# Optimization experiments

Measured on AMD Instinct MI355X. Metric: run time of the kernel, lower is better.

Reference implementation:

```python
import jax, jax.numpy as jnp
import numpy as np

NU = NI = 100_000  # nodes per ntype
E = 500_000        # edges per metapath graph
M = 2              # metapaths per ntype
D = 64             # in_size == out_size (num_heads = 1)
H = 128            # semantic-attention hidden
B = 8192           # batch of (user, pos, neg) indices
LRELU = 0.2        # DGL GATConv leaky-relu slope
EPS = 1e-5


def setup_inputs() -> dict:
    key = jax.random.key(0)
    ks = iter(jax.random.split(key, 40))
    rn = lambda sh, s=0.1: jax.random.normal(next(ks), sh, jnp.float32) * s
    ri = lambda sh, hi: jax.random.randint(next(ks), sh, 0, hi, jnp.int32)
    return dict(
        user_idx=ri((B,), NU), item_idx=ri((B,), NI), neg_item_idx=ri((B,), NI),
        user_feat=rn((NU, D), 1.0), item_feat=rn((NI, D), 1.0),
        u_src=ri((M, E), NU), u_dst=ri((M, E), NU),
        i_src=ri((M, E), NI), i_dst=ri((M, E), NI),
        u_W=rn((M, D, D)), u_al=rn((M, D)), u_ar=rn((M, D)), u_b=rn((M, D)),
        i_W=rn((M, D, D)), i_al=rn((M, D)), i_ar=rn((M, D)), i_b=rn((M, D)),
        u_saW1=rn((D, H)), u_sab1=rn((H,)), u_saW2=rn((H, 1)),
        i_saW1=rn((D, H)), i_sab1=rn((H,)), i_saW2=rn((H, 1)),
        userW=rn((D, D)), userb=rn((D,)), itemW=rn((D, D)), itemb=rn((D,)),
        ln_g=jnp.ones((D,), jnp.float32), ln_b=jnp.zeros((D,), jnp.float32),
    )


def _gat_stack(h, W, al, ar, b, src, dst, n_nodes):
    # One GATConv (single head) per metapath, vmapped over the metapath axis.
    def one(Wm, alm, arm, bm, s, d):
        feat = h @ Wm                               # (N, D)
        el = feat @ alm                             # (N,)
        er = feat @ arm                             # (N,)
        e = jax.nn.leaky_relu(el[s] + er[d], LRELU)  # (E,)
        m = jax.ops.segment_max(e, d, num_segments=n_nodes)
        ex = jnp.exp(e - m[d])
        den = jax.ops.segment_sum(ex, d, num_segments=n_nodes)
        alpha = ex / (den[d] + 1e-9)                # per-dst edge softmax
        out = jax.ops.segment_sum(alpha[:, None] * feat[s], d, num_segments=n_nodes)
        return jax.nn.elu(out + bm)                 # (N, D)
    return jax.vmap(one)(W, al, ar, b, src, dst)    # (M, N, D)


def _semantic_attention(z, W1, b1, W2):
    # z: (M, N, D) -> (N, D)
    w = jnp.mean(jnp.tanh(jnp.einsum('mnd,dh->mnh', z, W1) + b1) @ W2, axis=1)  # (M, 1)
    beta = jax.nn.softmax(w, axis=0)                 # softmax over metapaths
    return jnp.sum(beta[:, :, None] * z, axis=0)     # (N, D) -- beta (M,1)->(M,1,1)


def _layernorm(x, g, b):
    mu = x.mean(-1, keepdims=True)
    v = ((x - mu) ** 2).mean(-1, keepdims=True)
    return g * (x - mu) / jnp.sqrt(v + EPS) + b


def reference(user_idx, item_idx, neg_item_idx, user_feat, item_feat,
              u_src, u_dst, i_src, i_dst,
              u_W, u_al, u_ar, u_b, i_W, i_al, i_ar, i_b,
              u_saW1, u_sab1, u_saW2, i_saW1, i_sab1, i_saW2,
              userW, userb, itemW, itemb, ln_g, ln_b):
    zu = _gat_stack(user_feat, u_W, u_al, u_ar, u_b, u_src, u_dst, NU)
    zi = _gat_stack(item_feat, i_W, i_al, i_ar, i_b, i_src, i_dst, NI)
    user_emb = _semantic_attention(zu, u_saW1, u_sab1, u_saW2)
    item_emb = _semantic_attention(zi, i_saW1, i_sab1, i_saW2)
    user_emb = _layernorm(jax.nn.relu(user_emb @ userW + userb), ln_g, ln_b)
    item_emb = _layernorm(jax.nn.relu(item_emb @ itemW + itemb), ln_g, ln_b)
    return (user_emb[user_idx], item_emb[item_idx], item_emb[neg_item_idx])
```

## Files before the change

kernel.cpp:

```cpp
#include <hip/hip_runtime.h>
#include <math.h>

#define N_NODES 100000
#define N_EDGES 500000
#define BATCH   8192
#define NBLK    98
#define HISTX   512
#define FEATX   256

typedef __bf16 bf16;
typedef __bf16 bf16x8 __attribute__((ext_vector_type(8)));
typedef float  f32x4  __attribute__((ext_vector_type(4)));

#define MFMA16(a, b, c) __builtin_amdgcn_mfma_f32_16x16x32_bf16((a), (b), (c), 0, 0, 0)

__device__ __forceinline__ float wave_reduce_sum(float v) {
    #pragma unroll
    for (int off = 32; off; off >>= 1) v += __shfl_xor(v, off);
    return v;
}

__device__ __forceinline__ float fast_tanh(float x) {
    float e = __expf(2.f * x);
    return 1.f - 2.f / (e + 1.f);
}

__device__ __forceinline__ float b2f(unsigned short u) {
    return __int_as_float(((int)u) << 16);
}

__global__ void __launch_bounds__(256, 6)
fh_all(const float* __restrict__ uf, const float* __restrict__ itf,
       const float* __restrict__ uW, const float* __restrict__ iW,
       const float* __restrict__ ual, const float* __restrict__ ial,
       const float* __restrict__ uar, const float* __restrict__ iar,
       bf16* __restrict__ feat, float* __restrict__ el, float* __restrict__ er,
       const int* __restrict__ udst, const int* __restrict__ idst,
       int* __restrict__ cnt4, int* __restrict__ rank, int E, int N) {
    __shared__ bf16x8 ldsW[8][64];
    const int g = blockIdx.y;
    if (blockIdx.x < HISTX) {
        const int* dst = ((g < 2) ? udst : idst) + (size_t)(g & 1) * E;
        int* cntg = cnt4 + (size_t)g * N;
        int* rk = rank + (size_t)g * E;
        const int tid = blockIdx.x * blockDim.x + threadIdx.x;
        const int stride = HISTX * blockDim.x;
        for (int i0 = tid; i0 < E; i0 += 4 * stride) {
            const int i1 = i0 + stride, i2 = i0 + 2 * stride, i3 = i0 + 3 * stride;
            int d0 = dst[i0];
            int d1 = (i1 < E) ? dst[i1] : 0;
            int d2 = (i2 < E) ? dst[i2] : 0;
            int d3 = (i3 < E) ? dst[i3] : 0;
            int r0 = 0, r1 = 0, r2 = 0, r3 = 0;
            r0 = atomicAdd(&cntg[(size_t)(i0 & 3) * 4 * N + d0], 1);
            if (i1 < E) r1 = atomicAdd(&cntg[(size_t)(i1 & 3) * 4 * N + d1], 1);
            if (i2 < E) r2 = atomicAdd(&cntg[(size_t)(i2 & 3) * 4 * N + d2], 1);
            if (i3 < E) r3 = atomicAdd(&cntg[(size_t)(i3 & 3) * 4 * N + d3], 1);
            rk[i0] = r0;
            if (i1 < E) rk[i1] = r1;
            if (i2 < E) rk[i2] = r2;
            if (i3 < E) rk[i3] = r3;
        }
        return;
    }
    const int t = g >> 1, m = g & 1;
    const int fx = (int)blockIdx.x - HISTX;
    const float* h   = t ? itf : uf;
    const float* Wm  = (t ? iW : uW) + (size_t)m * 4096;
    const float* alb = (t ? ial : ual) + m * 64;
    const float* arb = (t ? iar : uar) + m * 64;
    for (int f = threadIdx.x; f < 8 * 64; f += blockDim.x) {
        int id = f >> 6, l = f & 63;
        int lc = l & 15, lq = l >> 4;
        int nt = id >> 1, kf = id & 1;
        bf16x8 v;
        #pragma unroll
        for (int j = 0; j < 8; ++j)
            v[j] = (bf16)Wm[(kf * 32 + lq * 8 + j) * 64 + nt * 16 + lc];
        ldsW[id][l] = v;
    }
    __syncthreads();
    const int lane = threadIdx.x & 63, wave = threadIdx.x >> 6, wpb = blockDim.x >> 6;
    const int c = lane & 15, q = lane >> 4;
    float alv[4], arv[4];
    #pragma unroll
    for (int nt = 0; nt < 4; ++nt) {
        alv[nt] = alb[nt * 16 + c];
        arv[nt] = arb[nt * 16 + c];
    }
    const f32x4 zf = {0.f, 0.f, 0.f, 0.f};
    const int tiles = N >> 4;
    bf16* fg   = feat + (size_t)g * N * 64;
    float* elg = el + (size_t)g * N;
    float* erg = er + (size_t)g * N;
    for (int tile = fx * wpb + wave; tile < tiles; tile += FEATX * wpb) {
        const float* hr = h + (size_t)(tile * 16 + c) * 64 + q * 8;
        f32x4 v0 = *(const f32x4*)hr;
        f32x4 v1 = *(const f32x4*)(hr + 4);
        f32x4 v2 = *(const f32x4*)(hr + 32);
        f32x4 v3 = *(const f32x4*)(hr + 36);
        bf16x8 a0, a1;
        #pragma unroll
        for (int j = 0; j < 4; ++j) {
            a0[j] = (bf16)v0[j]; a0[j + 4] = (bf16)v1[j];
            a1[j] = (bf16)v2[j]; a1[j + 4] = (bf16)v3[j];
        }
        f32x4 acc[4];
        #pragma unroll
        for (int nt = 0; nt < 4; ++nt) {
            acc[nt] = zf;
            acc[nt] = MFMA16(a0, ldsW[nt * 2][lane], acc[nt]);
            acc[nt] = MFMA16(a1, ldsW[nt * 2 + 1][lane], acc[nt]);
        }
        #pragma unroll
        for (int nt = 0; nt < 4; ++nt)
            #pragma unroll
            for (int r = 0; r < 4; ++r)
                fg[(size_t)(tile * 16 + q * 4 + r) * 64 + nt * 16 + c] = (bf16)acc[nt][r];
        #pragma unroll
        for (int r = 0; r < 4; ++r) {
            float se = 0.f, sr = 0.f;
            #pragma unroll
            for (int nt = 0; nt < 4; ++nt) {
                se = fmaf(acc[nt][r], alv[nt], se);
                sr = fmaf(acc[nt][r], arv[nt], sr);
            }
            #pragma unroll
            for (int off = 1; off < 16; off <<= 1) {
                se += __shfl_xor(se, off);
                sr += __shfl_xor(sr, off);
            }
            if (c == 0) {
                elg[tile * 16 + q * 4 + r] = se;
                erg[tile * 16 + q * 4 + r] = sr;
            }
        }
    }
}

__global__ void scanA(const int* __restrict__ cnt4, int* __restrict__ offsets,
                      int* __restrict__ bsum, int N) {
    const int g = blockIdx.y;
    const int* c = cnt4 + (size_t)g * N;
    int* o = offsets + (size_t)g * (N + 1);
    __shared__ int sh[1024];
    int i = blockIdx.x * 1024 + (int)threadIdx.x;
    int v = 0;
    if (i < N)
        v = c[i] + c[(size_t)4 * N + i] + c[(size_t)8 * N + i] + c[(size_t)12 * N + i];
    sh[threadIdx.x] = v;
    __syncthreads();
    for (int off = 1; off < 1024; off <<= 1) {
        int tv = (threadIdx.x >= (unsigned)off) ? sh[threadIdx.x - off] : 0;
        __syncthreads();
        sh[threadIdx.x] += tv;
        __syncthreads();
    }
    if (i < N) o[i] = sh[threadIdx.x] - v;
    if (threadIdx.x == 1023) bsum[g * 128 + blockIdx.x] = sh[1023];
}

__global__ void scanB(int* __restrict__ bsum, int* __restrict__ offsets,
                      float* __restrict__ wsum, int N) {
    const int g = blockIdx.y;
    int* bs = bsum + g * 128;
    __shared__ int sh[128];
    int tid = (int)threadIdx.x;
    if (g == 0 && tid < 4) wsum[tid] = 0.f;
    int v = (tid < NBLK) ? bs[tid] : 0;
    sh[tid] = v;
    __syncthreads();
    for (int off = 1; off < 128; off <<= 1) {
        int tv = (tid >= off) ? sh[tid - off] : 0;
        __syncthreads();
        sh[tid] += tv;
        __syncthreads();
    }
    if (tid < NBLK) bs[tid] = sh[tid] - v;
    if (tid == 0) offsets[(size_t)g * (N + 1) + N] = sh[127];
}

__global__ void scanC(int* __restrict__ offsets, int* __restrict__ off4,
                      const int* __restrict__ cnt4, const int* __restrict__ bsum, int N) {
    const int g = blockIdx.y;
    int i = blockIdx.x * blockDim.x + threadIdx.x;
    if (i < N) {
        int base = offsets[(size_t)g * (N + 1) + i] + bsum[g * 128 + (i >> 10)];
        offsets[(size_t)g * (N + 1) + i] = base;
        const int* c = cnt4 + (size_t)g * N;
        int c0 = c[i], c1 = c[(size_t)4 * N + i], c2 = c[(size_t)8 * N + i];
        int4 o;
        o.x = base; o.y = base + c0; o.z = base + c0 + c1; o.w = base + c0 + c1 + c2;
        *(int4*)(off4 + ((size_t)g * N + i) * 4) = o;
    }
}

__global__ void scatter_all(const int* __restrict__ usrc, const int* __restrict__ udst,
                            const int* __restrict__ isrc, const int* __restrict__ idst,
                            const float* __restrict__ el, const float* __restrict__ er,
                            const int* __restrict__ off4, const int* __restrict__ rank,
                            int2* __restrict__ epack, int E, int N) {
    const int g = blockIdx.y;
    const int* src = ((g < 2) ? usrc : isrc) + (size_t)(g & 1) * E;
    const int* dst = ((g < 2) ? udst : idst) + (size_t)(g & 1) * E;
    const float* elg = el + (size_t)g * N;
    const float* erg = er + (size_t)g * N;
    const int* o4 = off4 + (size_t)g * N * 4;
    const int* rk = rank + (size_t)g * E;
    int2* ep = epack + (size_t)g * E;
    const int tid = blockIdx.x * blockDim.x + threadIdx.x;
    const int stride = gridDim.x * blockDim.x;
    for (int i0 = tid; i0 < E; i0 += 4 * stride) {
        #pragma unroll
        for (int u = 0; u < 4; ++u) {
            const int i = i0 + u * stride;
            if (i < E) {
                int s = src[i], d = dst[i];
                int pos = o4[d * 4 + (i & 3)] + rk[i];
                float e = elg[s] + erg[d];
                e = (e >= 0.f) ? e : 0.2f * e;
                ep[pos] = make_int2(s << 7, __float_as_int(__expf(e)));
            }
        }
    }
}

__global__ void agg_all(const unsigned short* __restrict__ feat,
                        const float* __restrict__ ub, const float* __restrict__ ib,
                        const int* __restrict__ offsets, const int2* __restrict__ epack,
                        bf16* __restrict__ z, int E, int N) {
    const int g = blockIdx.y;
    const char* featg = (const char*)(feat + (size_t)g * N * 64);
    const float* bv = ((g < 2) ? ub : ib) + (g & 1) * 64;
    const int* offg = offsets + (size_t)g * (N + 1);
    const int2* ep = epack + (size_t)g * E;
    bf16* zg = z + (size_t)g * N * 64;
    const int lane = threadIdx.x & 63, wave = threadIdx.x >> 6, wpb = blockDim.x >> 6;
    const int lane2 = lane * 2;
    const float bl = bv[lane];
    for (int node0 = blockIdx.x * wpb + wave; node0 < N; node0 += gridDim.x * wpb) {
        const int node = __builtin_amdgcn_readfirstlane(node0);
        const int beg = __builtin_amdgcn_readfirstlane(offg[node]);
        const int end = __builtin_amdgcn_readfirstlane(offg[node + 1]);
        float l = 0.f, acc0 = 0.f, acc1 = 0.f;
        int i = beg;
        for (; i + 4 <= end; i += 4) {
            int2 p0 = ep[i], p1 = ep[i + 1], p2 = ep[i + 2], p3 = ep[i + 3];
            float f0 = b2f(*(const unsigned short*)(featg + (p0.x + lane2)));
            float f1 = b2f(*(const unsigned short*)(featg + (p1.x + lane2)));
            float f2 = b2f(*(const unsigned short*)(featg + (p2.x + lane2)));
            float f3 = b2f(*(const unsigned short*)(featg + (p3.x + lane2)));
            float w0 = __int_as_float(p0.y), w1 = __int_as_float(p1.y);
            float w2 = __int_as_float(p2.y), w3 = __int_as_float(p3.y);
            l += (w0 + w1) + (w2 + w3);
            acc0 = fmaf(w0, f0, acc0);
            acc1 = fmaf(w1, f1, acc1);
            acc0 = fmaf(w2, f2, acc0);
            acc1 = fmaf(w3, f3, acc1);
        }
        for (; i < end; ++i) {
            int2 p = ep[i];
            float w = __int_as_float(p.y);
            l += w;
            acc0 = fmaf(w, b2f(*(const unsigned short*)(featg + (p.x + lane2))), acc0);
        }
        float acc = acc0 + acc1;
        float o = acc / (l + 1e-9f);
        float zz = o + bl;
        zz = (zz > 0.f) ? zz : expm1f(zz);
        zg[(size_t)node * 64 + lane] = (bf16)zz;
    }
}

__global__ void __launch_bounds__(256, 4)
sem_mfma(const bf16* __restrict__ z,
         const float* __restrict__ uW1, const float* __restrict__ iW1,
         const float* __restrict__ ub1, const float* __restrict__ ib1,
         const float* __restrict__ uW2, const float* __restrict__ iW2,
         float* __restrict__ wsum, int N) {
    const int g = blockIdx.y, t = g >> 1;
    const float* W1 = t ? iW1 : uW1;
    const float* b1 = t ? ib1 : ub1;
    const float* W2 = t ? iW2 : uW2;
    __shared__ bf16x8 ldsW[16][64];
    for (int f = threadIdx.x; f < 16 * 64; f += blockDim.x) {
        int id = f >> 6, l = f & 63;
        int lc = l & 15, lq = l >> 4;
        int nt = id >> 1, kf = id & 1;
        bf16x8 v;
        #pragma unroll
        for (int j = 0; j < 8; ++j)
            v[j] = (bf16)W1[(kf * 32 + lq * 8 + j) * 128 + nt * 16 + lc];
        ldsW[id][l] = v;
    }
    __syncthreads();
    const int lane = threadIdx.x & 63, wave = threadIdx.x >> 6, wpb = blockDim.x >> 6;
    const int c = lane & 15, q = lane >> 4;
    float b1v[8], w2v[8];
    #pragma unroll
    for (int nt = 0; nt < 8; ++nt) { b1v[nt] = b1[nt * 16 + c]; w2v[nt] = W2[nt * 16 + c]; }
    const bf16* zg = z + (size_t)g * N * 64;
    const f32x4 zf = {0.f, 0.f, 0.f, 0.f};
    float local = 0.f;
    const int tiles = N >> 4;
    for (int tile = blockIdx.x * wpb + wave; tile < tiles; tile += gridDim.x * wpb) {
        const bf16* zr = zg + (size_t)(tile * 16 + c) * 64;
        bf16x8 a0 = *(const bf16x8*)(zr + q * 8);
        bf16x8 a1 = *(const bf16x8*)(zr + 32 + q * 8);
        f32x4 acc[8];
        #pragma unroll
        for (int nt = 0; nt < 8; ++nt) {
            acc[nt] = zf;
            acc[nt] = MFMA16(a0, ldsW[nt * 2][lane], acc[nt]);
            acc[nt] = MFMA16(a1, ldsW[nt * 2 + 1][lane], acc[nt]);
        }
        #pragma unroll
        for (int nt = 0; nt < 8; ++nt)
            #pragma unroll
            for (int r = 0; r < 4; ++r)
                local += w2v[nt] * fast_tanh(acc[nt][r] + b1v[nt]);
    }
    local = wave_reduce_sum(local);
    if (lane == 0) atomicAdd(&wsum[g], local);
}

__global__ void out_all(const int* __restrict__ uidx, const int* __restrict__ iidx,
                        const int* __restrict__ nidx, const bf16* __restrict__ z,
                        const float* __restrict__ wsum,
                        const float* __restrict__ userW, const float* __restrict__ userb,
                        const float* __restrict__ itemW, const float* __restrict__ itemb,
                        const float* __restrict__ ln_g, const float* __restrict__ ln_b,
                        float* __restrict__ out, int N, int B) {
    const int grp = blockIdx.y;
    const int t = (grp == 0) ? 0 : 1;
    const float* Wt = t ? itemW : userW;
    const float* bt = t ? itemb : userb;
    const int* idx = (grp == 0) ? uidx : ((grp == 1) ? iidx : nidx);
    const bf16* zg = z + (size_t)(t * 2) * N * 64;
    const int lane = threadIdx.x & 63, wave = threadIdx.x >> 6, wpb = blockDim.x >> 6;
    float Wc[64];
    #pragma unroll
    for (int k = 0; k < 64; ++k) Wc[k] = Wt[k * 64 + lane];
    const float btl = bt[lane], gl = ln_g[lane], lbl = ln_b[lane];
    const float invN = 1.f / (float)N;
    float w0 = wsum[t * 2] * invN, w1 = wsum[t * 2 + 1] * invN;
    float mx = fmaxf(w0, w1);
    float e0 = __expf(w0 - mx), e1 = __expf(w1 - mx);
    float bsum = e0 + e1;
    float beta0 = e0 / bsum, beta1 = e1 / bsum;
    for (int r = blockIdx.x * wpb + wave; r < B; r += gridDim.x * wpb) {
        const int urr = __builtin_amdgcn_readfirstlane(r);
        const int un = __builtin_amdgcn_readfirstlane(idx[urr]);
        float e = beta0 * (float)zg[(size_t)un * 64 + lane]
                + beta1 * (float)zg[(size_t)(N + un) * 64 + lane];
        float y = btl;
        #pragma unroll
        for (int k = 0; k < 64; ++k) y = fmaf(__shfl(e, k), Wc[k], y);
        y = fmaxf(y, 0.f);
        float mu = wave_reduce_sum(y) * (1.f / 64.f);
        float d = y - mu;
        float var = wave_reduce_sum(d * d) * (1.f / 64.f);
        out[(size_t)(grp * B + r) * 64 + lane] = gl * d / sqrtf(var + 1e-5f) + lbl;
    }
}

extern "C" void kernel_launch(void* const* d_in, const int* in_sizes, int n_in,
                              void* d_out, int out_size, void* d_ws, size_t ws_size,
                              hipStream_t stream) {
    const int* user_idx = (const int*)d_in[0];
    const int* item_idx = (const int*)d_in[1];
    const int* neg_idx  = (const int*)d_in[2];
    const float* user_feat = (const float*)d_in[3];
    const float* item_feat = (const float*)d_in[4];
    const int* u_src = (const int*)d_in[5];
    const int* u_dst = (const int*)d_in[6];
    const int* i_src = (const int*)d_in[7];
    const int* i_dst = (const int*)d_in[8];
    const float* u_W  = (const float*)d_in[9];
    const float* u_al = (const float*)d_in[10];
    const float* u_ar = (const float*)d_in[11];
    const float* u_b  = (const float*)d_in[12];
    const float* i_W  = (const float*)d_in[13];
    const float* i_al = (const float*)d_in[14];
    const float* i_ar = (const float*)d_in[15];
    const float* i_b  = (const float*)d_in[16];
    const float* u_saW1 = (const float*)d_in[17];
    const float* u_sab1 = (const float*)d_in[18];
    const float* u_saW2 = (const float*)d_in[19];
    const float* i_saW1 = (const float*)d_in[20];
    const float* i_sab1 = (const float*)d_in[21];
    const float* i_saW2 = (const float*)d_in[22];
    const float* userW = (const float*)d_in[23];
    const float* userb = (const float*)d_in[24];
    const float* itemW = (const float*)d_in[25];
    const float* itemb = (const float*)d_in[26];
    const float* ln_g  = (const float*)d_in[27];
    const float* ln_b  = (const float*)d_in[28];

    const int N = N_NODES, E = N_EDGES, B = BATCH;

    char* ws = (char*)d_ws;
    size_t off = 0;
    auto alloc = [&](size_t bytes) -> char* {
        char* p = ws + off;
        off += (bytes + 255) & ~(size_t)255;
        return p;
    };
    bf16* feat   = (bf16*)alloc((size_t)4 * N * 64 * 2);
    bf16* z      = (bf16*)alloc((size_t)4 * N * 64 * 2);
    float* el    = (float*)alloc((size_t)4 * N * 4);
    float* er    = (float*)alloc((size_t)4 * N * 4);
    int* offsets = (int*)alloc((size_t)4 * (N + 1) * 4);
    int* cnt4    = (int*)alloc((size_t)16 * N * 4);
    int* off4    = (int*)alloc((size_t)4 * N * 4 * 4);
    int* rank    = (int*)alloc((size_t)4 * E * 4);
    int2* epack  = (int2*)alloc((size_t)4 * E * 8);
    int* bsum    = (int*)alloc((size_t)4 * 128 * 4);
    float* wsum  = (float*)alloc(16);
    (void)ws_size; (void)in_sizes; (void)n_in; (void)out_size;

    dim3 blk(256);
    hipMemsetAsync(cnt4, 0, (size_t)16 * N * 4, stream);

    fh_all<<<dim3(HISTX + FEATX, 4), blk, 0, stream>>>(
        user_feat, item_feat, u_W, i_W, u_al, i_al, u_ar, i_ar,
        feat, el, er, u_dst, i_dst, cnt4, rank, E, N);
    scanA<<<dim3(NBLK, 4), dim3(1024), 0, stream>>>(cnt4, offsets, bsum, N);
    scanB<<<dim3(1, 4), dim3(128), 0, stream>>>(bsum, offsets, wsum, N);
    scanC<<<dim3(391, 4), blk, 0, stream>>>(offsets, off4, cnt4, bsum, N);
    scatter_all<<<dim3(1024, 4), blk, 0, stream>>>(u_src, u_dst, i_src, i_dst,
                                                   el, er, off4, rank, epack, E, N);
    agg_all<<<dim3(2048, 4), blk, 0, stream>>>((const unsigned short*)feat, u_b, i_b,
                                               offsets, epack, z, E, N);
    sem_mfma<<<dim3(256, 4), blk, 0, stream>>>(z, u_saW1, i_saW1, u_sab1, i_sab1,
                                               u_saW2, i_saW2, wsum, N);
    out_all<<<dim3(512, 3), blk, 0, stream>>>(user_idx, item_idx, neg_idx, z, wsum,
                                              userW, userb, itemW, itemb, ln_g, ln_b,
                                              (float*)d_out, N, B);
}
```

Measured before the change: 349.3 us.

## Fuse three-pass scan into single decoupled-lookback scan and drop sub-counters

Replaces the scanA/scanB/scanC chain with one scan kernel that uses decoupled lookback through a per-block status word, removing two kernel launches and the off4 table. The histogram goes back from four interleaved counter copies to a single counter per node, so scatter indexes offsets directly. This lowers launch count and memory traffic, but concentrates atomic contention on one counter per destination, and the lookback assumes earlier blocks make forward progress.

```diff
diff --git a/kernel.cpp b/kernel.cpp
--- a/kernel.cpp
+++ b/kernel.cpp
@@ -11,6 +11,7 @@
 typedef __bf16 bf16;
 typedef __bf16 bf16x8 __attribute__((ext_vector_type(8)));
 typedef float  f32x4  __attribute__((ext_vector_type(4)));
+typedef unsigned long long u64;
 
 #define MFMA16(a, b, c) __builtin_amdgcn_mfma_f32_16x16x32_bf16((a), (b), (c), 0, 0, 0)
 
@@ -36,12 +37,12 @@
        const float* __restrict__ uar, const float* __restrict__ iar,
        bf16* __restrict__ feat, float* __restrict__ el, float* __restrict__ er,
        const int* __restrict__ udst, const int* __restrict__ idst,
-       int* __restrict__ cnt4, int* __restrict__ rank, int E, int N) {
+       int* __restrict__ cnt, int* __restrict__ rank, int E, int N) {
     __shared__ bf16x8 ldsW[8][64];
     const int g = blockIdx.y;
     if (blockIdx.x < HISTX) {
         const int* dst = ((g < 2) ? udst : idst) + (size_t)(g & 1) * E;
-        int* cntg = cnt4 + (size_t)g * N;
+        int* cntg = cnt + (size_t)g * N;
         int* rk = rank + (size_t)g * E;
         const int tid = blockIdx.x * blockDim.x + threadIdx.x;
         const int stride = HISTX * blockDim.x;
@@ -52,10 +53,10 @@
             int d2 = (i2 < E) ? dst[i2] : 0;
             int d3 = (i3 < E) ? dst[i3] : 0;
             int r0 = 0, r1 = 0, r2 = 0, r3 = 0;
-            r0 = atomicAdd(&cntg[(size_t)(i0 & 3) * 4 * N + d0], 1);
-            if (i1 < E) r1 = atomicAdd(&cntg[(size_t)(i1 & 3) * 4 * N + d1], 1);
-            if (i2 < E) r2 = atomicAdd(&cntg[(size_t)(i2 & 3) * 4 * N + d2], 1);
-            if (i3 < E) r3 = atomicAdd(&cntg[(size_t)(i3 & 3) * 4 * N + d3], 1);
+            r0 = atomicAdd(&cntg[d0], 1);
+            if (i1 < E) r1 = atomicAdd(&cntg[d1], 1);
+            if (i2 < E) r2 = atomicAdd(&cntg[d2], 1);
+            if (i3 < E) r3 = atomicAdd(&cntg[d3], 1);
             rk[i0] = r0;
             if (i1 < E) rk[i1] = r1;
             if (i2 < E) rk[i2] = r2;
@@ -138,74 +139,65 @@
     }
 }
 
-__global__ void scanA(const int* __restrict__ cnt4, int* __restrict__ offsets,
-                      int* __restrict__ bsum, int N) {
-    const int g = blockIdx.y;
-    const int* c = cnt4 + (size_t)g * N;
-    int* o = offsets + (size_t)g * (N + 1);
+__global__ void __launch_bounds__(1024)
+scan_fused(const int* __restrict__ cnt, int* __restrict__ offsets,
+           u64* __restrict__ status, float* __restrict__ wsum, int N) {
+    const int g = blockIdx.y, b = blockIdx.x;
+    u64* stg = status + g * 128;
     __shared__ int sh[1024];
-    int i = blockIdx.x * 1024 + (int)threadIdx.x;
-    int v = 0;
-    if (i < N)
-        v = c[i] + c[(size_t)4 * N + i] + c[(size_t)8 * N + i] + c[(size_t)12 * N + i];
-    sh[threadIdx.x] = v;
+    __shared__ int total_s, excl_s;
+    const int tid = (int)threadIdx.x;
+    const int i = b * 1024 + tid;
+    int v = (i < N) ? cnt[(size_t)g * N + i] : 0;
+    sh[tid] = v;
     __syncthreads();
     for (int off = 1; off < 1024; off <<= 1) {
-        int tv = (threadIdx.x >= (unsigned)off) ? sh[threadIdx.x - off] : 0;
-        __syncthreads();
-        sh[threadIdx.x] += tv;
-        __syncthreads();
-    }
-    if (i < N) o[i] = sh[threadIdx.x] - v;
-    if (threadIdx.x == 1023) bsum[g * 128 + blockIdx.x] = sh[1023];
-}
-
-__global__ void scanB(int* __restrict__ bsum, int* __restrict__ offsets,
-                      float* __restrict__ wsum, int N) {
-    const int g = blockIdx.y;
-    int* bs = bsum + g * 128;
-    __shared__ int sh[128];
-    int tid = (int)threadIdx.x;
-    if (g == 0 && tid < 4) wsum[tid] = 0.f;
-    int v = (tid < NBLK) ? bs[tid] : 0;
-    sh[tid] = v;
-    __syncthreads();
-    for (int off = 1; off < 128; off <<= 1) {
         int tv = (tid >= off) ? sh[tid - off] : 0;
         __syncthreads();
         sh[tid] += tv;
         __syncthreads();
     }
-    if (tid < NBLK) bs[tid] = sh[tid] - v;
-    if (tid == 0) offsets[(size_t)g * (N + 1) + N] = sh[127];
-}
-
-__global__ void scanC(int* __restrict__ offsets, int* __restrict__ off4,
-                      const int* __restrict__ cnt4, const int* __restrict__ bsum, int N) {
-    const int g = blockIdx.y;
-    int i = blockIdx.x * blockDim.x + threadIdx.x;
-    if (i < N) {
-        int base = offsets[(size_t)g * (N + 1) + i] + bsum[g * 128 + (i >> 10)];
-        offsets[(size_t)g * (N + 1) + i] = base;
-        const int* c = cnt4 + (size_t)g * N;
-        int c0 = c[i], c1 = c[(size_t)4 * N + i], c2 = c[(size_t)8 * N + i];
-        int4 o;
-        o.x = base; o.y = base + c0; o.z = base + c0 + c1; o.w = base + c0 + c1 + c2;
-        *(int4*)(off4 + ((size_t)g * N + i) * 4) = o;
-    }
+    int incl = sh[tid];
+    if (tid == 1023) total_s = incl;
+    __syncthreads();
+    const int total = total_s;
+    if (tid == 0) {
+        if (b == 0) {
+            atomicExch(&stg[0], ((u64)total << 2) | 2ull);
+            excl_s = 0;
+        } else {
+            atomicExch(&stg[b], ((u64)total << 2) | 1ull);
+            int excl = 0, pb = b - 1;
+            while (true) {
+                u64 w = atomicAdd(&stg[pb], 0ull);
+                int st = (int)(w & 3ull);
+                if (st == 0) { __builtin_amdgcn_s_sleep(1); continue; }
+                excl += (int)(w >> 2);
+                if (st == 2) break;
+                --pb;
+            }
+            atomicExch(&stg[b], ((u64)(excl + total) << 2) | 2ull);
+            excl_s = excl;
+        }
+        if (b == 0 && g == 0) { wsum[0] = 0.f; wsum[1] = 0.f; wsum[2] = 0.f; wsum[3] = 0.f; }
+    }
+    __syncthreads();
+    const int excl = excl_s;
+    if (i < N) offsets[(size_t)g * (N + 1) + i] = excl + incl - v;
+    if (b == NBLK - 1 && tid == 1023) offsets[(size_t)g * (N + 1) + N] = excl + incl;
 }
 
 __global__ void scatter_all(const int* __restrict__ usrc, const int* __restrict__ udst,
                             const int* __restrict__ isrc, const int* __restrict__ idst,
                             const float* __restrict__ el, const float* __restrict__ er,
-                            const int* __restrict__ off4, const int* __restrict__ rank,
+                            const int* __restrict__ offsets, const int* __restrict__ rank,
                             int2* __restrict__ epack, int E, int N) {
     const int g = blockIdx.y;
     const int* src = ((g < 2) ? usrc : isrc) + (size_t)(g & 1) * E;
     const int* dst = ((g < 2) ? udst : idst) + (size_t)(g & 1) * E;
     const float* elg = el + (size_t)g * N;
     const float* erg = er + (size_t)g * N;
-    const int* o4 = off4 + (size_t)g * N * 4;
+    const int* offg = offsets + (size_t)g * (N + 1);
     const int* rk = rank + (size_t)g * E;
     int2* ep = epack + (size_t)g * E;
     const int tid = blockIdx.x * blockDim.x + threadIdx.x;
@@ -216,7 +208,7 @@
             const int i = i0 + u * stride;
             if (i < E) {
                 int s = src[i], d = dst[i];
-                int pos = o4[d * 4 + (i & 3)] + rk[i];
+                int pos = offg[d] + rk[i];
                 float e = elg[s] + erg[d];
                 e = (e >= 0.f) ? e : 0.2f * e;
                 ep[pos] = make_int2(s << 7, __float_as_int(__expf(e)));
@@ -411,25 +403,22 @@
     float* el    = (float*)alloc((size_t)4 * N * 4);
     float* er    = (float*)alloc((size_t)4 * N * 4);
     int* offsets = (int*)alloc((size_t)4 * (N + 1) * 4);
-    int* cnt4    = (int*)alloc((size_t)16 * N * 4);
-    int* off4    = (int*)alloc((size_t)4 * N * 4 * 4);
+    int* cnt     = (int*)alloc((size_t)4 * N * 4);
+    u64* status  = (u64*)alloc((size_t)4 * 128 * 8);
     int* rank    = (int*)alloc((size_t)4 * E * 4);
     int2* epack  = (int2*)alloc((size_t)4 * E * 8);
-    int* bsum    = (int*)alloc((size_t)4 * 128 * 4);
     float* wsum  = (float*)alloc(16);
     (void)ws_size; (void)in_sizes; (void)n_in; (void)out_size;
 
     dim3 blk(256);
-    hipMemsetAsync(cnt4, 0, (size_t)16 * N * 4, stream);
+    hipMemsetAsync(cnt, 0, (size_t)4 * N * 4 + 4096, stream);
 
     fh_all<<<dim3(HISTX + FEATX, 4), blk, 0, stream>>>(
         user_feat, item_feat, u_W, i_W, u_al, i_al, u_ar, i_ar,
-        feat, el, er, u_dst, i_dst, cnt4, rank, E, N);
-    scanA<<<dim3(NBLK, 4), dim3(1024), 0, stream>>>(cnt4, offsets, bsum, N);
-    scanB<<<dim3(1, 4), dim3(128), 0, stream>>>(bsum, offsets, wsum, N);
-    scanC<<<dim3(391, 4), blk, 0, stream>>>(offsets, off4, cnt4, bsum, N);
+        feat, el, er, u_dst, i_dst, cnt, rank, E, N);
+    scan_fused<<<dim3(NBLK, 4), dim3(1024), 0, stream>>>(cnt, offsets, status, wsum, N);
     scatter_all<<<dim3(1024, 4), blk, 0, stream>>>(u_src, u_dst, i_src, i_dst,
-                                                   el, er, off4, rank, epack, E, N);
+                                                   el, er, offsets, rank, epack, E, N);
     agg_all<<<dim3(2048, 4), blk, 0, stream>>>((const unsigned short*)feat, u_b, i_b,
                                                offsets, epack, z, E, N);
     sem_mfma<<<dim3(256, 4), blk, 0, stream>>>(z, u_saW1, i_saW1, u_sab1, i_sab1,
```

Result: faster. 338.8 us (-3.0%).
